# Performance work log

Hardware: AMD Instinct MI355X
Metric: run time of the kernel (lower is better)

The kernel has to match this reference:

```python
import jax, jax.numpy as jnp
import numpy as np

OUT_F = 4096
IN_F = 4096
NNZ_PER_ROW = 205            # ortho_ratio 0.05 * IN_F
NNZ = OUT_F * NNZ_PER_ROW    # 839680
ALPHA = 1.0                  # self.alpha (privacy on)


def setup_inputs() -> dict:
    key = jax.random.key(0)
    k1, k2, k3, k4 = jax.random.split(key, 4)
    x = jax.random.normal(k1, (4, 2048, IN_F), dtype=jnp.float32)
    # offset-uint8 quantized weight (stored here as int32 in [0,256))
    base_packed = jax.random.randint(k2, (OUT_F, IN_F), 0, 256, dtype=jnp.int32)
    # per-output-row dequant scales (robust_max/127 -> small positive values)
    scales = jax.random.uniform(k3, (OUT_F,), dtype=jnp.float32, minval=1e-4, maxval=4e-3)
    # CSR sparse residual: uniform row occupancy, sorted col indices per row
    ortho_vals = (jax.random.normal(k4, (NNZ,), dtype=jnp.float32) * 0.01).astype(jnp.float16)
    rng = np.random.default_rng(0)
    cols = np.sort(rng.integers(0, IN_F, size=(OUT_F, NNZ_PER_ROW)), axis=1)
    ortho_indices = jnp.asarray(cols.reshape(-1).astype(np.int32))
    ortho_ptr = jnp.asarray((np.arange(OUT_F + 1) * NNZ_PER_ROW).astype(np.int32))
    return {
        "x": x,
        "base_packed": base_packed,
        "scales": scales,
        "ortho_vals": ortho_vals,
        "ortho_indices": ortho_indices,
        "ortho_ptr": ortho_ptr,
    }


def reference(x, base_packed, scales, ortho_vals, ortho_indices, ortho_ptr):
    orig_shape = x.shape
    x_flat = x.reshape(-1, IN_F).astype(jnp.float32)          # [T, IN_F]
    # dequantize int8 base weight: (u8 - 128) * scale_row
    w_base = (base_packed.astype(jnp.float32) - 128.0) * scales[:, None]  # [OUT_F, IN_F]
    # expand CSR row pointers -> per-nnz row ids (fixed total length, jit-safe)
    counts = jnp.diff(ortho_ptr)
    rows = jnp.repeat(jnp.arange(OUT_F, dtype=jnp.int32), counts,
                      total_repeat_length=ortho_vals.shape[0])
    # scatter sparse residual into dense weight (matches torch CSR->dense fallback)
    w_ortho = jnp.zeros((OUT_F, IN_F), jnp.float32).at[rows, ortho_indices].add(
        ortho_vals.astype(jnp.float32))
    w = w_base + ALPHA * w_ortho
    out = x_flat @ w.T                                         # [T, OUT_F]
    return out.reshape(orig_shape[:-1] + (OUT_F,)).astype(x.dtype)
```

## Files before the change

kernel.cpp:

```cpp
#include <hip/hip_runtime.h>
#include <hip/hip_fp16.h>

#define IN_F 4096
#define OUT_F 4096
#define TOK 8192
#define NNZ_PER_ROW 205
#define NNZ (OUT_F * NNZ_PER_ROW)

typedef __attribute__((ext_vector_type(8))) _Float16 f16x8;
typedef __attribute__((ext_vector_type(4))) float floatx4;


__global__ __launch_bounds__(256) void cvt_x_kernel(const float* __restrict__ x,
                                                    _Float16* __restrict__ xh) {
    int t = blockIdx.x * 256 + threadIdx.x;
    const float4* p = (const float4*)x + (size_t)t * 2;
    float4 a = p[0], b = p[1];
    f16x8 h;
    h[0] = (_Float16)a.x; h[1] = (_Float16)a.y; h[2] = (_Float16)a.z; h[3] = (_Float16)a.w;
    h[4] = (_Float16)b.x; h[5] = (_Float16)b.y; h[6] = (_Float16)b.z; h[7] = (_Float16)b.w;
    ((f16x8*)xh)[t] = h;
}

__global__ __launch_bounds__(256) void dequant_w_kernel(const int* __restrict__ bp,
                                                        const float* __restrict__ scales,
                                                        _Float16* __restrict__ wh) {
    int t = blockIdx.x * 256 + threadIdx.x;
    int row = t >> 9;
    float s = scales[row];
    const int4* p = (const int4*)bp + (size_t)t * 2;
    int4 a = p[0], b = p[1];
    f16x8 h;
    h[0] = (_Float16)((float)(a.x - 128) * s);
    h[1] = (_Float16)((float)(a.y - 128) * s);
    h[2] = (_Float16)((float)(a.z - 128) * s);
    h[3] = (_Float16)((float)(a.w - 128) * s);
    h[4] = (_Float16)((float)(b.x - 128) * s);
    h[5] = (_Float16)((float)(b.y - 128) * s);
    h[6] = (_Float16)((float)(b.z - 128) * s);
    h[7] = (_Float16)((float)(b.w - 128) * s);
    ((f16x8*)wh)[t] = h;
}

__global__ __launch_bounds__(256) void sparse_add_kernel(const void* __restrict__ vals_raw,
                                                         const int* __restrict__ cols,
                                                         _Float16* __restrict__ wh) {
    int k = blockIdx.x * 256 + threadIdx.x;
    if (k >= NNZ) return;

    const float*    vf = (const float*)vals_raw;
    const _Float16* vh = (const _Float16*)vals_raw;
    float mx = 0.f;
    for (int i = 0; i < 64; ++i) {
        float a = __builtin_fabsf(vf[i]);
        mx = a > mx ? a : mx;
    }
    const bool is_f32 = (mx > 1e-6f) && (mx < 1.0f);

    int row  = k / NNZ_PER_ROW;
    int rbeg = row * NNZ_PER_ROW;
    int rend = rbeg + NNZ_PER_ROW;
    int c    = cols[k];
    if (k != rbeg && cols[k - 1] == c) return;

    float s = is_f32 ? vf[k] : (float)vh[k];
    for (int k2 = k + 1; k2 < rend && cols[k2] == c; ++k2)
        s += is_f32 ? vf[k2] : (float)vh[k2];

    _Float16* p = wh + (size_t)row * IN_F + c;
    *p = (_Float16)((float)*p + s);
}


__global__ __launch_bounds__(512, 2) void gemm256_kernel(const _Float16* __restrict__ X,
                                                         const _Float16* __restrict__ W,
                                                         float* __restrict__ out) {
    extern __shared__ char smem[];
    const int tid  = threadIdx.x;
    const int lane = tid & 63;
    const int w    = tid >> 6;
    const int wm   = w >> 2;
    const int wn   = w & 3;

    const int bid = blockIdx.x;
    const int swz = (bid & 7) * 64 + (bid >> 3);
    const int bm  = swz >> 4;
    const int bn  = swz & 15;

    const _Float16* Ap = X + (size_t)(bm * 256) * IN_F;
    const _Float16* Bp = W + (size_t)(bn * 256) * IN_F;

    int srow[2], sg[2];
#pragma unroll
    for (int j = 0; j < 2; ++j) {
        int ch  = w * 2 + j;
        int r   = ch * 16 + (lane >> 2);
        srow[j] = r;
        sg[j]   = (lane & 3) ^ ((r & 3) ^ ((r >> 2) & 3));
    }

    auto stage = [&](const _Float16* panel, int ldsOff, int kcol) {
#pragma unroll
        for (int j = 0; j < 2; ++j) {
            const _Float16* gp = panel + (size_t)srow[j] * IN_F + kcol + sg[j] * 8;
            char* lp = smem + ldsOff + (w * 2 + j) * 1024;
            __builtin_amdgcn_global_load_lds(
                (const __attribute__((address_space(1))) void*)gp,
                (__attribute__((address_space(3))) void*)lp, 16, 0, 0);
        }
    };

    const int q    = lane >> 4;
    const int r15  = lane & 15;
    const int slot = (q ^ ((r15 & 3) ^ ((r15 >> 2) & 3))) * 16;

    floatx4 acc[8][4] = {};
    f16x8 afrag[4], bfrag[4];

#define LOAD_B(KKH) do {                                                        \
    const char* Bb = smem + buf + 32768 + (KKH) * 16384;                        \
    _Pragma("unroll")                                                           \
    for (int nt = 0; nt < 4; ++nt)                                              \
        bfrag[nt] = *(const f16x8*)(Bb + (wn * 64 + nt * 16 + r15) * 64 + slot);\
} while (0)

#define LOAD_A(MQ, KKH) do {                                                    \
    const char* Ab = smem + buf + (KKH) * 16384;                                \
    _Pragma("unroll")                                                           \
    for (int mt = 0; mt < 4; ++mt)                                              \
        afrag[mt] = *(const f16x8*)(Ab + (wm * 128 + (MQ) * 64 + mt * 16 + r15) * 64 + slot);\
} while (0)

#define MFMA_BLK(MQ) do {                                                       \
    __builtin_amdgcn_s_setprio(1);                                              \
    _Pragma("unroll")                                                           \
    for (int mt = 0; mt < 4; ++mt)                                              \
        _Pragma("unroll")                                                       \
        for (int nt = 0; nt < 4; ++nt)                                          \
            acc[(MQ) * 4 + mt][nt] = __builtin_amdgcn_mfma_f32_16x16x32_f16(    \
                afrag[mt], bfrag[nt], acc[(MQ) * 4 + mt][nt], 0, 0, 0);         \
    __builtin_amdgcn_s_setprio(0);                                              \
} while (0)

    stage(Bp, 32768, 0);
    stage(Ap, 0, 0);
    stage(Bp, 49152, 32);
    stage(Ap, 16384, 32);
    stage(Bp, 65536 + 32768, 64);
    stage(Ap, 65536 + 0, 64);
    stage(Bp, 65536 + 49152, 96);
    asm volatile("s_waitcnt vmcnt(6)" ::: "memory");
    __builtin_amdgcn_s_barrier();

    for (int kt = 0; kt < 64; ++kt) {
        const int buf = (kt & 1) << 16;
        const int ks1 = kt + 1, ks2 = kt + 2;
        const int b1  = (ks1 & 1) << 16;
        const int b2  = (ks2 & 1) << 16;

        LOAD_B(0);
        LOAD_A(0, 0);
        if (ks1 < 64) stage(Ap, b1 + 16384, ks1 * 64 + 32);
        __builtin_amdgcn_s_barrier();
        MFMA_BLK(0);
        __builtin_amdgcn_s_barrier();

        LOAD_A(1, 0);
        if (ks2 < 64) stage(Bp, b2 + 32768, ks2 * 64);
        __builtin_amdgcn_s_barrier();
        MFMA_BLK(1);
        __builtin_amdgcn_s_barrier();

        LOAD_B(1);
        LOAD_A(0, 1);
        if (ks2 < 64) stage(Ap, b2, ks2 * 64);
        __builtin_amdgcn_s_barrier();
        MFMA_BLK(0);
        __builtin_amdgcn_s_barrier();

        LOAD_A(1, 1);
        if (ks2 < 64) stage(Bp, b2 + 49152, ks2 * 64 + 32);
        __builtin_amdgcn_s_barrier();
        MFMA_BLK(1);
        if (kt < 62)       asm volatile("s_waitcnt vmcnt(6)" ::: "memory");
        else if (kt == 62) asm volatile("s_waitcnt vmcnt(0)" ::: "memory");
        __builtin_amdgcn_s_barrier();
    }

#undef LOAD_B
#undef LOAD_A
#undef MFMA_BLK

#pragma unroll
    for (int mq = 0; mq < 2; ++mq)
#pragma unroll
        for (int mt = 0; mt < 4; ++mt)
#pragma unroll
            for (int nt = 0; nt < 4; ++nt) {
                const int o    = bn * 256 + wn * 64 + nt * 16 + r15;
                const int trow = bm * 256 + wm * 128 + mq * 64 + mt * 16 + q * 4;
                const floatx4 v = acc[mq * 4 + mt][nt];
#pragma unroll
                for (int r = 0; r < 4; ++r)
                    out[(size_t)(trow + r) * OUT_F + o] = v[r];
            }
}


__global__ __launch_bounds__(256) void gemm_fast_kernel(const _Float16* __restrict__ X,
                                                        const _Float16* __restrict__ W,
                                                        float* __restrict__ out) {
    __shared__ __align__(1024) char smem[32768];
    const int tid  = threadIdx.x;
    const int lane = tid & 63;
    const int w    = tid >> 6;
    const int wm   = w >> 1;
    const int wn   = w & 1;
    const int bm   = blockIdx.y;
    const int bn   = blockIdx.x;

    const int l8 = lane >> 3;
    const int ls = lane & 7;
    const int e  = ls ^ l8;

    floatx4 acc[4][4] = {};

    for (int k0 = 0; k0 < IN_F; k0 += 64) {
#pragma unroll
        for (int j = 0; j < 4; ++j) {
            int c   = w * 4 + j;
            int row = c * 8 + l8;
            const _Float16* gp = X + ((size_t)(bm * 128 + row)) * IN_F + k0 + e * 8;
            char* lp = smem + c * 1024;
            __builtin_amdgcn_global_load_lds((const __attribute__((address_space(1))) void*)gp,
                                             (__attribute__((address_space(3))) void*)lp,
                                             16, 0, 0);
        }
#pragma unroll
        for (int j = 0; j < 4; ++j) {
            int c   = w * 4 + j;
            int row = c * 8 + l8;
            const _Float16* gp = W + ((size_t)(bn * 128 + row)) * IN_F + k0 + e * 8;
            char* lp = smem + 16384 + c * 1024;
            __builtin_amdgcn_global_load_lds((const __attribute__((address_space(1))) void*)gp,
                                             (__attribute__((address_space(3))) void*)lp,
                                             16, 0, 0);
        }
        __syncthreads();

        const int q   = lane >> 4;
        const int r15 = lane & 15;
#pragma unroll
        for (int kk = 0; kk < 64; kk += 32) {
            int j = (kk >> 3) + q;
            f16x8 a[4], b[4];
#pragma unroll
            for (int mt = 0; mt < 4; ++mt) {
                int row = wm * 64 + mt * 16 + r15;
                a[mt] = *(const f16x8*)(smem + row * 128 + ((j ^ (row & 7)) * 16));
            }
#pragma unroll
            for (int nt = 0; nt < 4; ++nt) {
                int row = wn * 64 + nt * 16 + r15;
                b[nt] = *(const f16x8*)(smem + 16384 + row * 128 + ((j ^ (row & 7)) * 16));
            }
#pragma unroll
            for (int mt = 0; mt < 4; ++mt)
#pragma unroll
                for (int nt = 0; nt < 4; ++nt)
                    acc[mt][nt] = __builtin_amdgcn_mfma_f32_16x16x32_f16(a[mt], b[nt],
                                                                         acc[mt][nt], 0, 0, 0);
        }
        __syncthreads();
    }

    const int q   = lane >> 4;
    const int r15 = lane & 15;
#pragma unroll
    for (int mt = 0; mt < 4; ++mt)
#pragma unroll
        for (int nt = 0; nt < 4; ++nt) {
            int o     = bn * 128 + wn * 64 + nt * 16 + r15;
            int tbase = bm * 128 + wm * 64 + mt * 16 + q * 4;
#pragma unroll
            for (int r = 0; r < 4; ++r)
                out[(size_t)(tbase + r) * OUT_F + o] = acc[mt][nt][r];
        }
}

__global__ __launch_bounds__(256) void gemm_kernel(const float* __restrict__ X,
                                                   const _Float16* __restrict__ W,
                                                   float* __restrict__ out) {
    __shared__ __align__(16) _Float16 As[128 * 72];
    __shared__ __align__(16) _Float16 Bs[128 * 72];
    const int tid  = threadIdx.x;
    const int lane = tid & 63;
    const int w    = tid >> 6;
    const int wm   = w >> 1;
    const int wn   = w & 1;
    const int bm   = blockIdx.y;
    const int bn   = blockIdx.x;
    const int srow = tid >> 3;
    const int sch  = tid & 7;

    const float*    Xb = X + (size_t)(bm * 128) * IN_F;
    const _Float16* Wb = W + (size_t)(bn * 128) * IN_F;

    floatx4 acc[4][4] = {};

    for (int k0 = 0; k0 < IN_F; k0 += 64) {
#pragma unroll
        for (int p = 0; p < 4; ++p) {
            int row = p * 32 + srow;
            const float* gp = Xb + (size_t)row * IN_F + k0 + sch * 8;
            float4 u = ((const float4*)gp)[0];
            float4 v = ((const float4*)gp)[1];
            f16x8 h;
            h[0] = (_Float16)u.x; h[1] = (_Float16)u.y;
            h[2] = (_Float16)u.z; h[3] = (_Float16)u.w;
            h[4] = (_Float16)v.x; h[5] = (_Float16)v.y;
            h[6] = (_Float16)v.z; h[7] = (_Float16)v.w;
            *(f16x8*)&As[row * 72 + sch * 8] = h;
        }
#pragma unroll
        for (int p = 0; p < 4; ++p) {
            int row = p * 32 + srow;
            *(f16x8*)&Bs[row * 72 + sch * 8] =
                *(const f16x8*)(Wb + (size_t)row * IN_F + k0 + sch * 8);
        }
        __syncthreads();

        const int q   = lane >> 4;
        const int r15 = lane & 15;
#pragma unroll
        for (int kk = 0; kk < 64; kk += 32) {
            int j = (kk >> 3) + q;
            f16x8 a[4], b[4];
#pragma unroll
            for (int mt = 0; mt < 4; ++mt) {
                int row = wm * 64 + mt * 16 + r15;
                a[mt] = *(const f16x8*)&As[row * 72 + j * 8];
            }
#pragma unroll
            for (int nt = 0; nt < 4; ++nt) {
                int row = wn * 64 + nt * 16 + r15;
                b[nt] = *(const f16x8*)&Bs[row * 72 + j * 8];
            }
#pragma unroll
            for (int mt = 0; mt < 4; ++mt)
#pragma unroll
                for (int nt = 0; nt < 4; ++nt)
                    acc[mt][nt] = __builtin_amdgcn_mfma_f32_16x16x32_f16(a[mt], b[nt],
                                                                         acc[mt][nt], 0, 0, 0);
        }
        __syncthreads();
    }

    const int q   = lane >> 4;
    const int r15 = lane & 15;
#pragma unroll
    for (int mt = 0; mt < 4; ++mt)
#pragma unroll
        for (int nt = 0; nt < 4; ++nt) {
            int o     = bn * 128 + wn * 64 + nt * 16 + r15;
            int tbase = bm * 128 + wm * 64 + mt * 16 + q * 4;
#pragma unroll
            for (int r = 0; r < 4; ++r)
                out[(size_t)(tbase + r) * OUT_F + o] = acc[mt][nt][r];
        }
}


extern "C" void kernel_launch(void* const* d_in, const int* in_sizes, int n_in,
                              void* d_out, int out_size, void* d_ws, size_t ws_size,
                              hipStream_t stream) {
    const float* x      = (const float*)d_in[0];
    const int*   bp     = (const int*)d_in[1];
    const float* scales = (const float*)d_in[2];
    const void*  vals   = (const void*)d_in[3];
    const int*   cols   = (const int*)d_in[4];
    float*       out    = (float*)d_out;

    _Float16* wh = (_Float16*)d_ws;
    const size_t wh_bytes = (size_t)OUT_F * IN_F * 2;
    const size_t xh_bytes = (size_t)TOK * IN_F * 2;

    static int use256 = -1;
    if (use256 < 0) {
        hipError_t e = hipFuncSetAttribute((const void*)gemm256_kernel,
                                           hipFuncAttributeMaxDynamicSharedMemorySize,
                                           131072);
        use256 = (e == hipSuccess) ? 1 : 0;
    }

    dequant_w_kernel<<<OUT_F * IN_F / 8 / 256, 256, 0, stream>>>(bp, scales, wh);
    sparse_add_kernel<<<(NNZ + 255) / 256, 256, 0, stream>>>(vals, cols, wh);

    if (ws_size >= wh_bytes + xh_bytes) {
        _Float16* xh = (_Float16*)((char*)d_ws + wh_bytes);
        cvt_x_kernel<<<TOK * IN_F / 8 / 256, 256, 0, stream>>>(x, xh);
        if (use256) {
            gemm256_kernel<<<dim3(512), 512, 131072, stream>>>(xh, wh, out);
        } else {
            dim3 grid(OUT_F / 128, TOK / 128);
            gemm_fast_kernel<<<grid, 256, 0, stream>>>(xh, wh, out);
        }
    } else {
        dim3 grid(OUT_F / 128, TOK / 128);
        gemm_kernel<<<grid, 256, 0, stream>>>(x, wh, out);
    }
}
```

Measured before the change: 539.6 us.

## Restage GEMM LDS tiles as 128-byte rows with XOR swizzle and reorder prefetch

Changes the shared-memory tile layout from two 32-wide K halves (64-byte rows) to a single 64-wide K row of 128 bytes per matrix row. Each global load now covers 8 rows with 8 contiguous 16-byte chunks, using a simpler lane-XOR swizzle, which gives longer contiguous global reads and a different bank-conflict pattern. The prefetch schedule is rearranged: A for the next K-tile is staged in the first two phases, B two tiles ahead is staged in the last phase, and the vmcnt wait thresholds are adjusted to match. This risks new LDS bank conflicts or pipeline hazards if the wait counts do not line up with the new issue order.

New measurement: 524.0 us. -2.9%, faster.

```diff
diff --git a/kernel.cpp b/kernel.cpp
--- a/kernel.cpp
+++ b/kernel.cpp
@@ -90,45 +90,42 @@
     const _Float16* Ap = X + (size_t)(bm * 256) * IN_F;
     const _Float16* Bp = W + (size_t)(bn * 256) * IN_F;
 
-    int srow[2], sg[2];
-#pragma unroll
-    for (int j = 0; j < 2; ++j) {
-        int ch  = w * 2 + j;
-        int r   = ch * 16 + (lane >> 2);
-        srow[j] = r;
-        sg[j]   = (lane & 3) ^ ((r & 3) ^ ((r >> 2) & 3));
-    }
-
-    auto stage = [&](const _Float16* panel, int ldsOff, int kcol) {
+    const int l8 = lane >> 3;
+    const int e  = (lane & 7) ^ l8;
+
+    auto stage = [&](const _Float16* panel, int ldsBase, int rowBase, int kcol) {
 #pragma unroll
         for (int j = 0; j < 2; ++j) {
-            const _Float16* gp = panel + (size_t)srow[j] * IN_F + kcol + sg[j] * 8;
-            char* lp = smem + ldsOff + (w * 2 + j) * 1024;
+            int ch = w * 2 + j;
+            const _Float16* gp = panel + (size_t)(rowBase + ch * 8 + l8) * IN_F + kcol + e * 8;
+            char* lp = smem + ldsBase + ch * 1024;
             __builtin_amdgcn_global_load_lds(
                 (const __attribute__((address_space(1))) void*)gp,
                 (__attribute__((address_space(3))) void*)lp, 16, 0, 0);
         }
     };
 
-    const int q    = lane >> 4;
-    const int r15  = lane & 15;
-    const int slot = (q ^ ((r15 & 3) ^ ((r15 >> 2) & 3))) * 16;
+    const int q     = lane >> 4;
+    const int r15   = lane & 15;
+    const int slot0 = (q ^ (r15 & 7)) * 16;
 
     floatx4 acc[8][4] = {};
     f16x8 afrag[4], bfrag[4];
 
 #define LOAD_B(KKH) do {                                                        \
-    const char* Bb = smem + buf + 32768 + (KKH) * 16384;                        \
+    const char* Bb = smem + buf + 32768;                                        \
     _Pragma("unroll")                                                           \
     for (int nt = 0; nt < 4; ++nt)                                              \
-        bfrag[nt] = *(const f16x8*)(Bb + (wn * 64 + nt * 16 + r15) * 64 + slot);\
+        bfrag[nt] = *(const f16x8*)(Bb + (wn * 64 + nt * 16 + r15) * 128        \
+                                       + (slot0 ^ ((KKH) * 64)));               \
 } while (0)
 
 #define LOAD_A(MQ, KKH) do {                                                    \
-    const char* Ab = smem + buf + (KKH) * 16384;                                \
+    const char* Ab = smem + buf;                                                \
     _Pragma("unroll")                                                           \
     for (int mt = 0; mt < 4; ++mt)                                              \
-        afrag[mt] = *(const f16x8*)(Ab + (wm * 128 + (MQ) * 64 + mt * 16 + r15) * 64 + slot);\
+        afrag[mt] = *(const f16x8*)(Ab + (wm * 128 + (MQ) * 64 + mt * 16 + r15) * 128 \
+                                       + (slot0 ^ ((KKH) * 64)));               \
 } while (0)
 
 #define MFMA_BLK(MQ) do {                                                       \
@@ -142,47 +139,46 @@
     __builtin_amdgcn_s_setprio(0);                                              \
 } while (0)
 
-    stage(Bp, 32768, 0);
-    stage(Ap, 0, 0);
-    stage(Bp, 49152, 32);
-    stage(Ap, 16384, 32);
-    stage(Bp, 65536 + 32768, 64);
-    stage(Ap, 65536 + 0, 64);
-    stage(Bp, 65536 + 49152, 96);
-    asm volatile("s_waitcnt vmcnt(6)" ::: "memory");
+    stage(Bp, 32768, 0, 0);
+    stage(Bp, 49152, 128, 0);
+    stage(Ap, 0, 0, 0);
+    stage(Ap, 16384, 128, 0);
+    stage(Bp, 65536 + 32768, 0, 64);
+    stage(Bp, 65536 + 49152, 128, 64);
+    asm volatile("s_waitcnt vmcnt(4)" ::: "memory");
     __builtin_amdgcn_s_barrier();
 
     for (int kt = 0; kt < 64; ++kt) {
         const int buf = (kt & 1) << 16;
-        const int ks1 = kt + 1, ks2 = kt + 2;
-        const int b1  = (ks1 & 1) << 16;
-        const int b2  = (ks2 & 1) << 16;
+        const int ob  = ((kt + 1) & 1) << 16;
 
         LOAD_B(0);
         LOAD_A(0, 0);
-        if (ks1 < 64) stage(Ap, b1 + 16384, ks1 * 64 + 32);
+        if (kt < 63) stage(Ap, ob, 0, (kt + 1) * 64);
         __builtin_amdgcn_s_barrier();
         MFMA_BLK(0);
         __builtin_amdgcn_s_barrier();
 
         LOAD_A(1, 0);
-        if (ks2 < 64) stage(Bp, b2 + 32768, ks2 * 64);
+        if (kt < 63) stage(Ap, ob + 16384, 128, (kt + 1) * 64);
         __builtin_amdgcn_s_barrier();
         MFMA_BLK(1);
         __builtin_amdgcn_s_barrier();
 
         LOAD_B(1);
         LOAD_A(0, 1);
-        if (ks2 < 64) stage(Ap, b2, ks2 * 64);
         __builtin_amdgcn_s_barrier();
         MFMA_BLK(0);
         __builtin_amdgcn_s_barrier();
 
         LOAD_A(1, 1);
-        if (ks2 < 64) stage(Bp, b2 + 49152, ks2 * 64 + 32);
+        if (kt < 62) {
+            stage(Bp, buf + 32768, 0, (kt + 2) * 64);
+            stage(Bp, buf + 49152, 128, (kt + 2) * 64);
+        }
         __builtin_amdgcn_s_barrier();
         MFMA_BLK(1);
-        if (kt < 62)       asm volatile("s_waitcnt vmcnt(6)" ::: "memory");
+        if (kt < 62)       asm volatile("s_waitcnt vmcnt(4)" ::: "memory");
         else if (kt == 62) asm volatile("s_waitcnt vmcnt(0)" ::: "memory");
         __builtin_amdgcn_s_barrier();
     }
```
